# Kernel optimization log

Hardware: AMD Instinct MI355X
Metric: run time of the kernel (lower is better)

The kernel has to match this reference:

```python
import jax, jax.numpy as jnp
import numpy as np

B, L, D = 2, 2048, 1024
H = 16          # num_heads
HD = D // H     # head_dim = 64
NEG_INF = jnp.float32(-1e30)


def setup_inputs() -> dict:
    key = jax.random.key(0)
    ks = jax.random.split(key, 10)
    s = 1.0 / np.sqrt(D)
    return {
        "x": jax.random.normal(ks[0], (B, L, D), dtype=jnp.float32),
        "Wq": jax.random.normal(ks[1], (D, D), dtype=jnp.float32) * s,
        "bq": jnp.zeros((D,), jnp.float32),
        "Wk": jax.random.normal(ks[2], (D, D), dtype=jnp.float32) * s,
        "bk": jnp.zeros((D,), jnp.float32),
        "Wv": jax.random.normal(ks[3], (D, D), dtype=jnp.float32) * s,
        "bv": jnp.zeros((D,), jnp.float32),
        "Wo": jax.random.normal(ks[4], (D, D), dtype=jnp.float32) * s,
        "bo": jnp.zeros((D,), jnp.float32),
        "local_scale": jnp.ones((1,), jnp.float32),
        "global_scale": jnp.ones((1,), jnp.float32),
    }


def reference(x, Wq, bq, Wk, bk, Wv, bv, Wo, bo, local_scale, global_scale):
    # projections -> [B, H, L, HD]
    def proj(W, b):
        return (x @ W + b).reshape(B, L, H, HD).transpose(0, 2, 1, 3)
    Q, K, V = proj(Wq, bq), proj(Wk, bk), proj(Wv, bv)
    lh = H // 2
    inv_sqrt = 1.0 / jnp.sqrt(jnp.float32(HD))

    # local (causal) heads
    scores_l = jnp.einsum("bhqd,bhkd->bhqk", Q[:, :lh], K[:, :lh]) * inv_sqrt
    causal = jnp.tril(jnp.ones((L, L), dtype=bool))  # keep lower triangle
    scores_l = jnp.where(causal, scores_l * local_scale, NEG_INF)
    attn_local = jax.nn.softmax(scores_l, axis=-1)
    out_local = jnp.einsum("bhqk,bhkd->bhqd", attn_local, V[:, :lh])

    # global (full) heads
    scores_g = jnp.einsum("bhqd,bhkd->bhqk", Q[:, lh:], K[:, lh:]) * inv_sqrt
    attn_global = jax.nn.softmax(scores_g * global_scale, axis=-1)
    out_global = jnp.einsum("bhqk,bhkd->bhqd", attn_global, V[:, lh:])

    out = jnp.concatenate([out_local, out_global], axis=1)  # [B,H,L,HD]
    out = out.transpose(0, 2, 1, 3).reshape(B, L, D)
    out = out @ Wo + bo
    return (out, attn_local, attn_global)
```

## Files before the change

### kernel.cpp

```cpp
#include <hip/hip_runtime.h>
#include <hip/hip_bf16.h>

#define B 2
#define L 2048
#define D 1024
#define H 16
#define HD 64
#define LH 8
#define NEG_INF -1e30f

typedef __hip_bfloat16 bf16;
typedef unsigned short ushort_t;
typedef short bf16x8 __attribute__((ext_vector_type(8)));
typedef unsigned short us8 __attribute__((ext_vector_type(8)));
typedef float f32x4 __attribute__((ext_vector_type(4)));

#define MFMA16(a, b, c) __builtin_amdgcn_mfma_f32_16x16x32_bf16((a), (b), (c), 0, 0, 0)

#define WAITBAR(N) do {                                              \
    asm volatile("s_waitcnt vmcnt(" #N ") lgkmcnt(0)" ::: "memory"); \
    __builtin_amdgcn_sched_barrier(0);                               \
    __builtin_amdgcn_s_barrier();                                    \
  } while (0)

#if defined(__has_builtin)
#if __has_builtin(__builtin_amdgcn_global_load_lds)
#define HAVE_GLOAD_LDS 1
#endif
#endif

template<typename T> struct IsF32;
template<> struct IsF32<float> { static constexpr int value = 1; };
template<> struct IsF32<bf16>  { static constexpr int value = 0; };

__device__ __forceinline__ float ldf(const float* p, size_t i) { return p[i]; }
__device__ __forceinline__ float ldf(const bf16* p, size_t i) { return __bfloat162float(p[i]); }

__device__ __forceinline__ float4 ld4(const float* p, size_t i) {
  return *reinterpret_cast<const float4*>(p + i);
}
__device__ __forceinline__ float4 ld4(const bf16* p, size_t i) {
  ushort4 u = *reinterpret_cast<const ushort4*>(p + i);
  float4 f;
  f.x = __uint_as_float(((unsigned)u.x) << 16);
  f.y = __uint_as_float(((unsigned)u.y) << 16);
  f.z = __uint_as_float(((unsigned)u.z) << 16);
  f.w = __uint_as_float(((unsigned)u.w) << 16);
  return f;
}
__device__ __forceinline__ ushort_t bfh(float v) {
  bf16 h = __float2bfloat16(v);
  return *reinterpret_cast<ushort_t*>(&h);
}
__device__ __forceinline__ float bf2f(ushort_t u) {
  return __uint_as_float(((unsigned)u) << 16);
}
__device__ __forceinline__ void stf(float* p, size_t i, float v) { p[i] = v; }
__device__ __forceinline__ void stf(bf16* p, size_t i, float v) { p[i] = __float2bfloat16(v); }

__device__ __forceinline__ int swz(int row, int slot) {
  return row * 64 + (((slot ^ (row & 7)) & 7) << 3);
}
__device__ __forceinline__ int swzc(int row, int c) {
  return row * 64 + (((((c >> 3) ^ row) & 7) << 3) | (c & 7));
}

#if defined(HAVE_GLOAD_LDS)
__device__ __forceinline__ void gload_lds16(const ushort_t* src, ushort_t* dst) {
  __builtin_amdgcn_global_load_lds(
      (const __attribute__((address_space(1))) unsigned int*)src,
      (__attribute__((address_space(3))) unsigned int*)dst, 16, 0, 0);
}
#endif

__device__ __forceinline__ void stage64(const ushort_t* g, size_t gstride,
                                        ushort_t* lds, int w, int ln) {
  #pragma unroll
  for (int c = 0; c < 2; ++c) {
    const int row = 16 * w + 8 * c + (ln >> 3);
    const int slot = ((ln & 7) ^ row) & 7;
    const ushort_t* src = g + (size_t)row * gstride + slot * 8;
#if defined(HAVE_GLOAD_LDS)
    gload_lds16(src, lds + (size_t)(16 * w + 8 * c) * 64);
#else
    *reinterpret_cast<uint4*>(&lds[row * 64 + (ln & 7) * 8]) =
        *reinterpret_cast<const uint4*>(src);
#endif
  }
}

__device__ __forceinline__ void stage128(const ushort_t* g, ushort_t* lds,
                                         int w, int ln) {
  #pragma unroll
  for (int c = 0; c < 4; ++c) {
    const int row = 32 * w + 8 * c + (ln >> 3);
    const int slot = ((ln & 7) ^ row) & 7;
    const ushort_t* src = g + (size_t)row * 1024 + slot * 8;
#if defined(HAVE_GLOAD_LDS)
    gload_lds16(src, lds + (size_t)(32 * w + 8 * c) * 64);
#else
    *reinterpret_cast<uint4*>(&lds[row * 64 + (ln & 7) * 8]) =
        *reinterpret_cast<const uint4*>(src);
#endif
  }
}

__global__ void detect_dtype_kernel(const unsigned short* __restrict__ x,
                                    int* __restrict__ flag) {
  int bad = 0;
  for (int i = threadIdx.x; i < 1024; i += 64) {
    if (((x[i] >> 7) & 0xFF) >= 170) bad = 1;
  }
  unsigned long long m = __ballot(bad);
  if (threadIdx.x == 0) *flag = (m != 0ULL) ? 1 : 0;
}

__global__ __launch_bounds__(256)
void cast_f32_kernel(const int* __restrict__ flag, int want,
                     const float* __restrict__ in,
                     ushort_t* __restrict__ hp, int n4) {
  if (*flag != want) return;
  int i = blockIdx.x * 256 + threadIdx.x;
  const int stride = gridDim.x * 256;
  for (; i < n4; i += stride) {
    float4 v = *reinterpret_cast<const float4*>(in + 4 * (size_t)i);
    ushort4 h;
    h.x = bfh(v.x); h.y = bfh(v.y); h.z = bfh(v.z); h.w = bfh(v.w);
    *reinterpret_cast<ushort4*>(hp + 4 * (size_t)i) = h;
  }
}

template<typename T>
__global__ __launch_bounds__(256)
void transW_kernel(const int* __restrict__ flag,
                   const T* __restrict__ W0, const T* __restrict__ W1,
                   const T* __restrict__ W2, const T* __restrict__ W3,
                   ushort_t* __restrict__ base, ushort_t* __restrict__ baseWo) {
  if (*flag != IsF32<T>::value) return;
  const int z = blockIdx.z;
  const T* W = z == 0 ? W0 : (z == 1 ? W1 : (z == 2 ? W2 : W3));
  ushort_t* hp = (z < 3) ? (base + (size_t)z * 2097152) : baseWo;
  __shared__ float ts[64][69];
  const int k0 = blockIdx.x * 64, n0 = blockIdx.y * 64;
  const int t = threadIdx.x;
  #pragma unroll
  for (int p = 0; p < 4; ++p) {
    int r = p * 16 + (t >> 4);
    int c = (t & 15) * 4;
    float4 v = ld4(W, (size_t)(k0 + r) * D + n0 + c);
    ts[r][c] = v.x; ts[r][c + 1] = v.y; ts[r][c + 2] = v.z; ts[r][c + 3] = v.w;
  }
  __syncthreads();
  #pragma unroll
  for (int p = 0; p < 4; ++p) {
    int n = p * 16 + (t >> 4);
    int k4 = (t & 15) * 4;
    ushort4 h;
    h.x = bfh(ts[k4][n]);
    h.y = bfh(ts[k4 + 1][n]);
    h.z = bfh(ts[k4 + 2][n]);
    h.w = bfh(ts[k4 + 3][n]);
    *reinterpret_cast<ushort4*>(&hp[(size_t)(n0 + n) * D + k0 + k4]) = h;
  }
}

template<typename T>
__global__ __launch_bounds__(256, 3)
void gemm_kernel(const int* __restrict__ flag,
                 const ushort_t* __restrict__ xA, const ushort_t* __restrict__ aoh,
                 const ushort_t* __restrict__ wbase, const ushort_t* __restrict__ woT,
                 const T* __restrict__ bq, const T* __restrict__ bk,
                 const T* __restrict__ bv, const T* __restrict__ bo,
                 ushort_t* __restrict__ qh, ushort_t* __restrict__ ql,
                 ushort_t* __restrict__ kh, ushort_t* __restrict__ kl,
                 ushort_t* __restrict__ vth, T* __restrict__ out0, int zfix) {
  if (*flag != IsF32<T>::value) return;
  const int cpx = gridDim.x >> 3;
  const int swzid = ((int)blockIdx.x & 7) * cpx + ((int)blockIdx.x >> 3);
  const int mtile = swzid & 31;
  const int ntile = (swzid >> 5) & 15;
  const int z = (zfix >= 0) ? zfix : (swzid >> 9);
  const int m0 = mtile * 128, n0 = ntile * 64;

  const bool isOut = (z == 3);
  const ushort_t* Ah = isOut ? aoh : xA;
  const ushort_t* wh = isOut ? woT : (wbase + (size_t)z * 2097152);

  __shared__ ushort_t As[2][8192], Bs[2][4096];

  const int ln = threadIdx.x & 63, w = threadIdx.x >> 6;
  const int m = ln & 15, hi = ln >> 4;

  f32x4 acc[2][4] = {};

  stage128(Ah + (size_t)m0 * 1024, As[0], w, ln);
  stage64(wh + (size_t)n0 * 1024, 1024, Bs[0], w, ln);
  __syncthreads();
  for (int step = 0; step < 16; ++step) {
    const int cur = step & 1;
    if (step < 15) {
      stage128(Ah + (size_t)m0 * 1024 + (step + 1) * 64, As[cur ^ 1], w, ln);
      stage64(wh + (size_t)n0 * 1024 + (step + 1) * 64, 1024, Bs[cur ^ 1], w, ln);
    }
    __builtin_amdgcn_s_setprio(1);
    #pragma unroll
    for (int kc = 0; kc < 2; ++kc) {
      bf16x8 a_h[2], b_h[4];
      #pragma unroll
      for (int f = 0; f < 2; ++f)
        a_h[f] = *reinterpret_cast<const bf16x8*>(&As[cur][swz(w * 32 + f * 16 + m, kc * 4 + hi)]);
      #pragma unroll
      for (int f = 0; f < 4; ++f)
        b_h[f] = *reinterpret_cast<const bf16x8*>(&Bs[cur][swz(f * 16 + m, kc * 4 + hi)]);
      #pragma unroll
      for (int fr = 0; fr < 2; ++fr)
        #pragma unroll
        for (int fc = 0; fc < 4; ++fc)
          acc[fr][fc] = MFMA16(a_h[fr], b_h[fc], acc[fr][fc]);
    }
    __builtin_amdgcn_s_setprio(0);
    __syncthreads();
  }

  #pragma unroll
  for (int fc = 0; fc < 4; ++fc) {
    const int col = n0 + fc * 16 + m;
    if (isOut) {
      const float bv_ = ldf(bo, (size_t)col);
      #pragma unroll
      for (int fr = 0; fr < 2; ++fr)
        #pragma unroll
        for (int r = 0; r < 4; ++r) {
          const int tok = m0 + w * 32 + fr * 16 + 4 * hi + r;
          stf(out0, (size_t)tok * D + col, acc[fr][fc][r] + bv_);
        }
    } else if (z == 2) {
      const int hh = col >> 6, d = col & 63;
      const float bv_ = ldf(bv, (size_t)col);
      #pragma unroll
      for (int fr = 0; fr < 2; ++fr) {
        const int tok0 = m0 + w * 32 + fr * 16 + 4 * hi;
        const int bb = tok0 >> 11, ll = tok0 & (L - 1);
        ushort4 hv;
        hv.x = bfh(acc[fr][fc][0] + bv_);
        hv.y = bfh(acc[fr][fc][1] + bv_);
        hv.z = bfh(acc[fr][fc][2] + bv_);
        hv.w = bfh(acc[fr][fc][3] + bv_);
        *reinterpret_cast<ushort4*>(
            &vth[((size_t)(bb * H + hh) * HD + d) * L + ll]) = hv;
      }
    } else {
      const int hh = col >> 6, d = col & 63;
      const float bv_ = ldf(z == 0 ? bq : bk, (size_t)col);
      ushort_t* oh = z == 0 ? qh : kh;
      ushort_t* ol = z == 0 ? ql : kl;
      #pragma unroll
      for (int fr = 0; fr < 2; ++fr)
        #pragma unroll
        for (int r = 0; r < 4; ++r) {
          const int tok = m0 + w * 32 + fr * 16 + 4 * hi + r;
          const int bb = tok >> 11, ll = tok & (L - 1);
          const float v = acc[fr][fc][r] + bv_;
          const size_t o = ((size_t)(bb * H + hh) * L + ll) * HD + d;
          const ushort_t hu = bfh(v);
          oh[o] = hu; ol[o] = bfh(v - bf2f(hu));
        }
    }
  }
}

template<typename T>
__global__ __launch_bounds__(256, 3)
void attn_kernel(const int* __restrict__ flag,
                 const ushort_t* __restrict__ Qh_g, const ushort_t* __restrict__ Ql_g,
                 const ushort_t* __restrict__ Kh_g, const ushort_t* __restrict__ Kl_g,
                 const ushort_t* __restrict__ Vth_g,
                 const T* __restrict__ lsp, const T* __restrict__ gsp,
                 T* __restrict__ attn_l, T* __restrict__ attn_g,
                 ushort_t* __restrict__ AOh) {
  if (*flag != IsF32<T>::value) return;
  const int bid = blockIdx.x;
  const int xcd = bid & 7, slot = bid >> 3;
  const int bhg = xcd + 8 * (slot >> 5);
  const int strip_raw = slot & 31;
  const int bb = bhg >> 4, h = bhg & 15;
  const bool is_local = h < LH;
  const int strip = is_local ? (31 - strip_raw) : strip_raw;
  const int q0 = strip * 64;
  const int ln = threadIdx.x & 63, w = threadIdx.x >> 6;
  const int m = ln & 15, hi = ln >> 4;

  const float cscale =
      (is_local ? ldf(lsp, (size_t)0) : ldf(gsp, (size_t)0)) * 0.125f;
  const size_t bh_off = ((size_t)bb * H + h) * L * HD;
  const ushort_t* Qhb = Qh_g + bh_off;
  const ushort_t* Qlb = Ql_g + bh_off;
  const ushort_t* Khb = Kh_g + bh_off;
  const ushort_t* Klb = Kl_g + bh_off;
  const ushort_t* Vhb = Vth_g + bh_off;

  __shared__ ushort_t KsH[2][4096], KsL[2][4096], VsH[4096], Ps[4096];

  bf16x8 qfh[2], qfl[2];
  {
    const size_t qb = (size_t)(q0 + 16 * w + m) * HD + hi * 8;
    qfh[0] = *reinterpret_cast<const bf16x8*>(Qhb + qb);
    qfh[1] = *reinterpret_cast<const bf16x8*>(Qhb + qb + 32);
    qfl[0] = *reinterpret_cast<const bf16x8*>(Qlb + qb);
    qfl[1] = *reinterpret_cast<const bf16x8*>(Qlb + qb + 32);
  }

  float m_ = NEG_INF, l_ = 0.f;
  const int nkt = is_local ? (strip + 1) : (L / 64);
  T* aout = is_local ? attn_l : attn_g;
  const size_t arow0 =
      ((size_t)(bb * LH + (is_local ? h : h - LH)) * L + q0) * L;

  stage64(Khb, HD, KsH[0], w, ln);
  __syncthreads();
  for (int kt = 0; kt < nkt; ++kt) {
    const int cur = kt & 1;
    if (kt + 1 < nkt)
      stage64(Khb + (size_t)((kt + 1) * 64) * HD, HD, KsH[cur ^ 1], w, ln);

    f32x4 s[4] = {};
    __builtin_amdgcn_s_setprio(1);
    #pragma unroll
    for (int nt = 0; nt < 4; ++nt) {
      #pragma unroll
      for (int kc = 0; kc < 2; ++kc) {
        bf16x8 kbh = *reinterpret_cast<const bf16x8*>(&KsH[cur][swz(nt * 16 + m, kc * 4 + hi)]);
        s[nt] = MFMA16(kbh, qfh[kc], s[nt]);
      }
    }
    __builtin_amdgcn_s_setprio(0);

    const bool dg = is_local && (kt == strip);
    #pragma unroll
    for (int nt = 0; nt < 4; ++nt)
      #pragma unroll
      for (int r = 0; r < 4; ++r) {
        float v = s[nt][r] * cscale;
        if (dg && (nt * 16 + 4 * hi + r > 16 * w + m)) v = NEG_INF;
        s[nt][r] = v;
      }

    float tm = NEG_INF;
    #pragma unroll
    for (int nt = 0; nt < 4; ++nt)
      #pragma unroll
      for (int r = 0; r < 4; ++r) tm = fmaxf(tm, s[nt][r]);
    tm = fmaxf(tm, __shfl_xor(tm, 16, 64));
    tm = fmaxf(tm, __shfl_xor(tm, 32, 64));
    const float mn = fmaxf(m_, tm);
    float sum = 0.f;
    #pragma unroll
    for (int nt = 0; nt < 4; ++nt)
      #pragma unroll
      for (int r = 0; r < 4; ++r) sum += __expf(s[nt][r] - mn);
    sum += __shfl_xor(sum, 16, 64);
    sum += __shfl_xor(sum, 32, 64);
    l_ = l_ * __expf(m_ - mn) + sum;
    m_ = mn;
    __syncthreads();
  }

  const float invl = 1.0f / l_;
  f32x4 o_[4] = {};

  stage64(Khb, HD, KsH[0], w, ln);
  stage64(Klb, HD, KsL[0], w, ln);
  __syncthreads();
  for (int kt = 0; kt < nkt; ++kt) {
    const int cur = kt & 1;
    const bool pf = (kt + 1 < nkt);
    stage64(Vhb + (size_t)(kt * 64), L, VsH, w, ln);
    if (pf) {
      stage64(Khb + (size_t)((kt + 1) * 64) * HD, HD, KsH[cur ^ 1], w, ln);
      stage64(Klb + (size_t)((kt + 1) * 64) * HD, HD, KsL[cur ^ 1], w, ln);
    }

    f32x4 s[4] = {};
    __builtin_amdgcn_s_setprio(1);
    #pragma unroll
    for (int nt = 0; nt < 4; ++nt) {
      #pragma unroll
      for (int kc = 0; kc < 2; ++kc) {
        bf16x8 kbh = *reinterpret_cast<const bf16x8*>(&KsH[cur][swz(nt * 16 + m, kc * 4 + hi)]);
        bf16x8 kbl = *reinterpret_cast<const bf16x8*>(&KsL[cur][swz(nt * 16 + m, kc * 4 + hi)]);
        s[nt] = MFMA16(kbh, qfh[kc], s[nt]);
        s[nt] = MFMA16(kbl, qfh[kc], s[nt]);
        s[nt] = MFMA16(kbh, qfl[kc], s[nt]);
      }
    }
    __builtin_amdgcn_s_setprio(0);

    const bool dg = is_local && (kt == strip);
    #pragma unroll
    for (int nt = 0; nt < 4; ++nt) {
      float v0 = s[nt][0] * cscale, v1 = s[nt][1] * cscale;
      float v2 = s[nt][2] * cscale, v3 = s[nt][3] * cscale;
      if (dg) {
        const int kbq = nt * 16 + 4 * hi, qq = 16 * w + m;
        if (kbq + 0 > qq) v0 = NEG_INF;
        if (kbq + 1 > qq) v1 = NEG_INF;
        if (kbq + 2 > qq) v2 = NEG_INF;
        if (kbq + 3 > qq) v3 = NEG_INF;
      }
      ushort4 pk;
      pk.x = bfh(__expf(v0 - m_) * invl);
      pk.y = bfh(__expf(v1 - m_) * invl);
      pk.z = bfh(__expf(v2 - m_) * invl);
      pk.w = bfh(__expf(v3 - m_) * invl);
      *reinterpret_cast<ushort4*>(&Ps[swzc(16 * w + m, nt * 16 + 4 * hi)]) = pk;
    }
    if (pf) { WAITBAR(4); } else { WAITBAR(0); }

    __builtin_amdgcn_s_setprio(1);
    bf16x8 pf0 = *reinterpret_cast<const bf16x8*>(&Ps[swz(16 * w + m, hi)]);
    bf16x8 pf1 = *reinterpret_cast<const bf16x8*>(&Ps[swz(16 * w + m, 4 + hi)]);
    #pragma unroll
    for (int dt = 0; dt < 4; ++dt) {
      bf16x8 vf0 = *reinterpret_cast<const bf16x8*>(&VsH[swz(dt * 16 + m, hi)]);
      bf16x8 vf1 = *reinterpret_cast<const bf16x8*>(&VsH[swz(dt * 16 + m, 4 + hi)]);
      o_[dt] = MFMA16(pf0, vf0, o_[dt]);
      o_[dt] = MFMA16(pf1, vf1, o_[dt]);
    }
    __builtin_amdgcn_s_setprio(0);

    {
      const int pr = 16 * w + (ln >> 2);
      const int cs = (ln & 3) * 2;
      us8 v0 = *reinterpret_cast<const us8*>(&Ps[swz(pr, cs)]);
      us8 v1 = *reinterpret_cast<const us8*>(&Ps[swz(pr, cs + 1)]);
      const size_t gi = arow0 + (size_t)pr * L + (size_t)(kt * 64 + (ln & 3) * 16);
      if constexpr (IsF32<T>::value) {
        float* dst = (float*)aout + gi;
        *reinterpret_cast<float4*>(dst + 0) =
            make_float4(bf2f(v0[0]), bf2f(v0[1]), bf2f(v0[2]), bf2f(v0[3]));
        *reinterpret_cast<float4*>(dst + 4) =
            make_float4(bf2f(v0[4]), bf2f(v0[5]), bf2f(v0[6]), bf2f(v0[7]));
        *reinterpret_cast<float4*>(dst + 8) =
            make_float4(bf2f(v1[0]), bf2f(v1[1]), bf2f(v1[2]), bf2f(v1[3]));
        *reinterpret_cast<float4*>(dst + 12) =
            make_float4(bf2f(v1[4]), bf2f(v1[5]), bf2f(v1[6]), bf2f(v1[7]));
      } else {
        bf16* dst = (bf16*)aout + gi;
        *reinterpret_cast<uint4*>(dst + 0) = *reinterpret_cast<const uint4*>(&v0);
        *reinterpret_cast<uint4*>(dst + 8) = *reinterpret_cast<const uint4*>(&v1);
      }
    }
    WAITBAR(4);
  }

  if (is_local) {
    const int pr = 16 * w + (ln >> 2);
    const size_t rbase = arow0 + (size_t)pr * L;
    for (int c = nkt * 64 + (ln & 3) * 16; c < L; c += 64) {
      if constexpr (IsF32<T>::value) {
        float* dst = (float*)aout + rbase + c;
        const float4 z4 = make_float4(0.f, 0.f, 0.f, 0.f);
        *reinterpret_cast<float4*>(dst + 0) = z4;
        *reinterpret_cast<float4*>(dst + 4) = z4;
        *reinterpret_cast<float4*>(dst + 8) = z4;
        *reinterpret_cast<float4*>(dst + 12) = z4;
      } else {
        bf16* dst = (bf16*)aout + rbase + c;
        const uint4 z4 = make_uint4(0u, 0u, 0u, 0u);
        *reinterpret_cast<uint4*>(dst + 0) = z4;
        *reinterpret_cast<uint4*>(dst + 8) = z4;
      }
    }
  }

  #pragma unroll
  for (int dt = 0; dt < 4; ++dt)
    #pragma unroll
    for (int r = 0; r < 4; ++r)
      AOh[((size_t)bb * L + q0 + 16 * w + 4 * hi + r) * D + h * HD + dt * 16 + m] =
          bfh(o_[dt][r]);
}

template<typename T>
static void launch_path(void* const* d_in, void* d_out, void* d_ws, hipStream_t stream) {
  const int want = IsF32<T>::value;
  const int* flag = (const int*)d_ws;
  ushort_t* Qh  = (ushort_t*)((char*)d_ws + 256);
  ushort_t* Ql  = Qh + 4194304;
  ushort_t* Kh  = Ql + 4194304;
  ushort_t* Kl  = Kh + 4194304;
  ushort_t* Vth = Kl + 4194304;
  ushort_t* AOh = Vth + 4194304;
  ushort_t* Woth = AOh + 4194304;

  const T* x  = (const T*)d_in[0];
  const T* Wq = (const T*)d_in[1];
  const T* bq = (const T*)d_in[2];
  const T* Wk = (const T*)d_in[3];
  const T* bk = (const T*)d_in[4];
  const T* Wv = (const T*)d_in[5];
  const T* bv = (const T*)d_in[6];
  const T* Wo = (const T*)d_in[7];
  const T* bo = (const T*)d_in[8];
  const T* ls = (const T*)d_in[9];
  const T* gs = (const T*)d_in[10];

  T* out0   = (T*)d_out;
  T* attn_l = out0 + (size_t)B * L * D;
  T* attn_g = attn_l + (size_t)B * LH * L * L;
  ushort_t* xh  = (ushort_t*)attn_g;
  ushort_t* Wt3 = xh + 4194304;

  if constexpr (IsF32<T>::value)
    cast_f32_kernel<<<1024, 256, 0, stream>>>(flag, want, (const float*)x, xh, 1048576);
  transW_kernel<T><<<dim3(16, 16, 4), 256, 0, stream>>>(
      flag, Wq, Wk, Wv, Wo, Wt3, Woth);
  const ushort_t* xA = IsF32<T>::value ? xh : (const ushort_t*)x;

  gemm_kernel<T><<<1536, 256, 0, stream>>>(
      flag, xA, AOh, Wt3, Woth, bq, bk, bv, bo,
      Qh, Ql, Kh, Kl, Vth, out0, -1);
  attn_kernel<T><<<1024, 256, 0, stream>>>(
      flag, Qh, Ql, Kh, Kl, Vth, ls, gs, attn_l, attn_g, AOh);
  gemm_kernel<T><<<512, 256, 0, stream>>>(
      flag, xA, AOh, Wt3, Woth, bq, bk, bv, bo,
      Qh, Ql, Kh, Kl, Vth, out0, 3);
}

extern "C" void kernel_launch(void* const* d_in, const int* in_sizes, int n_in,
                              void* d_out, int out_size, void* d_ws, size_t ws_size,
                              hipStream_t stream) {
  int* flag = (int*)d_ws;
  detect_dtype_kernel<<<1, 64, 0, stream>>>((const unsigned short*)d_in[0], flag);
  launch_path<float>(d_in, d_out, d_ws, stream);
  launch_path<bf16>(d_in, d_out, d_ws, stream);
}
```

Baseline: 921.1 us.

## Shrink GEMM M-tile to 64 and double-batch K tiles in attention stats pass

The projection GEMMs now use 64x64 tiles instead of 128x64, doubling the grid size and lowering LDS and register use per block; launch bounds are raised to 5 blocks per SM. The attention kernel's shared memory is merged into one aliased buffer. Its first (row-max/sum) pass now stages two K tiles per barrier, halving synchronisations in that pass. Smaller GEMM tiles cut A/B reuse per MFMA, adding more global and LDS traffic in exchange for occupancy.

```diff
diff --git a/kernel.cpp b/kernel.cpp
--- a/kernel.cpp
+++ b/kernel.cpp
@@ -82,22 +82,6 @@
     const ushort_t* src = g + (size_t)row * gstride + slot * 8;
 #if defined(HAVE_GLOAD_LDS)
     gload_lds16(src, lds + (size_t)(16 * w + 8 * c) * 64);
-#else
-    *reinterpret_cast<uint4*>(&lds[row * 64 + (ln & 7) * 8]) =
-        *reinterpret_cast<const uint4*>(src);
-#endif
-  }
-}
-
-__device__ __forceinline__ void stage128(const ushort_t* g, ushort_t* lds,
-                                         int w, int ln) {
-  #pragma unroll
-  for (int c = 0; c < 4; ++c) {
-    const int row = 32 * w + 8 * c + (ln >> 3);
-    const int slot = ((ln & 7) ^ row) & 7;
-    const ushort_t* src = g + (size_t)row * 1024 + slot * 8;
-#if defined(HAVE_GLOAD_LDS)
-    gload_lds16(src, lds + (size_t)(32 * w + 8 * c) * 64);
 #else
     *reinterpret_cast<uint4*>(&lds[row * 64 + (ln & 7) * 8]) =
         *reinterpret_cast<const uint4*>(src);
@@ -165,7 +149,7 @@
 }
 
 template<typename T>
-__global__ __launch_bounds__(256, 3)
+__global__ __launch_bounds__(256, 5)
 void gemm_kernel(const int* __restrict__ flag,
                  const ushort_t* __restrict__ xA, const ushort_t* __restrict__ aoh,
                  const ushort_t* __restrict__ wbase, const ushort_t* __restrict__ woT,
@@ -177,46 +161,42 @@
   if (*flag != IsF32<T>::value) return;
   const int cpx = gridDim.x >> 3;
   const int swzid = ((int)blockIdx.x & 7) * cpx + ((int)blockIdx.x >> 3);
-  const int mtile = swzid & 31;
-  const int ntile = (swzid >> 5) & 15;
-  const int z = (zfix >= 0) ? zfix : (swzid >> 9);
-  const int m0 = mtile * 128, n0 = ntile * 64;
+  const int mtile = swzid & 63;
+  const int ntile = (swzid >> 6) & 15;
+  const int z = (zfix >= 0) ? zfix : (swzid >> 10);
+  const int m0 = mtile * 64, n0 = ntile * 64;
 
   const bool isOut = (z == 3);
   const ushort_t* Ah = isOut ? aoh : xA;
   const ushort_t* wh = isOut ? woT : (wbase + (size_t)z * 2097152);
 
-  __shared__ ushort_t As[2][8192], Bs[2][4096];
+  __shared__ ushort_t As[2][4096], Bs[2][4096];
 
   const int ln = threadIdx.x & 63, w = threadIdx.x >> 6;
   const int m = ln & 15, hi = ln >> 4;
 
-  f32x4 acc[2][4] = {};
-
-  stage128(Ah + (size_t)m0 * 1024, As[0], w, ln);
+  f32x4 acc[4] = {};
+
+  stage64(Ah + (size_t)m0 * 1024, 1024, As[0], w, ln);
   stage64(wh + (size_t)n0 * 1024, 1024, Bs[0], w, ln);
   __syncthreads();
   for (int step = 0; step < 16; ++step) {
     const int cur = step & 1;
     if (step < 15) {
-      stage128(Ah + (size_t)m0 * 1024 + (step + 1) * 64, As[cur ^ 1], w, ln);
+      stage64(Ah + (size_t)m0 * 1024 + (step + 1) * 64, 1024, As[cur ^ 1], w, ln);
       stage64(wh + (size_t)n0 * 1024 + (step + 1) * 64, 1024, Bs[cur ^ 1], w, ln);
     }
     __builtin_amdgcn_s_setprio(1);
     #pragma unroll
     for (int kc = 0; kc < 2; ++kc) {
-      bf16x8 a_h[2], b_h[4];
-      #pragma unroll
-      for (int f = 0; f < 2; ++f)
-        a_h[f] = *reinterpret_cast<const bf16x8*>(&As[cur][swz(w * 32 + f * 16 + m, kc * 4 + hi)]);
+      bf16x8 a_h = *reinterpret_cast<const bf16x8*>(&As[cur][swz(16 * w + m, kc * 4 + hi)]);
+      bf16x8 b_h[4];
       #pragma unroll
       for (int f = 0; f < 4; ++f)
         b_h[f] = *reinterpret_cast<const bf16x8*>(&Bs[cur][swz(f * 16 + m, kc * 4 + hi)]);
       #pragma unroll
-      for (int fr = 0; fr < 2; ++fr)
-        #pragma unroll
-        for (int fc = 0; fc < 4; ++fc)
-          acc[fr][fc] = MFMA16(a_h[fr], b_h[fc], acc[fr][fc]);
+      for (int fc = 0; fc < 4; ++fc)
+        acc[fc] = MFMA16(a_h, b_h[fc], acc[fc]);
     }
     __builtin_amdgcn_s_setprio(0);
     __syncthreads();
@@ -228,43 +208,36 @@
     if (isOut) {
       const float bv_ = ldf(bo, (size_t)col);
       #pragma unroll
-      for (int fr = 0; fr < 2; ++fr)
-        #pragma unroll
-        for (int r = 0; r < 4; ++r) {
-          const int tok = m0 + w * 32 + fr * 16 + 4 * hi + r;
-          stf(out0, (size_t)tok * D + col, acc[fr][fc][r] + bv_);
-        }
+      for (int r = 0; r < 4; ++r) {
+        const int tok = m0 + 16 * w + 4 * hi + r;
+        stf(out0, (size_t)tok * D + col, acc[fc][r] + bv_);
+      }
     } else if (z == 2) {
       const int hh = col >> 6, d = col & 63;
       const float bv_ = ldf(bv, (size_t)col);
-      #pragma unroll
-      for (int fr = 0; fr < 2; ++fr) {
-        const int tok0 = m0 + w * 32 + fr * 16 + 4 * hi;
-        const int bb = tok0 >> 11, ll = tok0 & (L - 1);
-        ushort4 hv;
-        hv.x = bfh(acc[fr][fc][0] + bv_);
-        hv.y = bfh(acc[fr][fc][1] + bv_);
-        hv.z = bfh(acc[fr][fc][2] + bv_);
-        hv.w = bfh(acc[fr][fc][3] + bv_);
-        *reinterpret_cast<ushort4*>(
-            &vth[((size_t)(bb * H + hh) * HD + d) * L + ll]) = hv;
-      }
+      const int tok0 = m0 + 16 * w + 4 * hi;
+      const int bb = tok0 >> 11, ll = tok0 & (L - 1);
+      ushort4 hv;
+      hv.x = bfh(acc[fc][0] + bv_);
+      hv.y = bfh(acc[fc][1] + bv_);
+      hv.z = bfh(acc[fc][2] + bv_);
+      hv.w = bfh(acc[fc][3] + bv_);
+      *reinterpret_cast<ushort4*>(
+          &vth[((size_t)(bb * H + hh) * HD + d) * L + ll]) = hv;
     } else {
       const int hh = col >> 6, d = col & 63;
       const float bv_ = ldf(z == 0 ? bq : bk, (size_t)col);
       ushort_t* oh = z == 0 ? qh : kh;
       ushort_t* ol = z == 0 ? ql : kl;
       #pragma unroll
-      for (int fr = 0; fr < 2; ++fr)
-        #pragma unroll
-        for (int r = 0; r < 4; ++r) {
-          const int tok = m0 + w * 32 + fr * 16 + 4 * hi + r;
-          const int bb = tok >> 11, ll = tok & (L - 1);
-          const float v = acc[fr][fc][r] + bv_;
-          const size_t o = ((size_t)(bb * H + hh) * L + ll) * HD + d;
-          const ushort_t hu = bfh(v);
-          oh[o] = hu; ol[o] = bfh(v - bf2f(hu));
-        }
+      for (int r = 0; r < 4; ++r) {
+        const int tok = m0 + 16 * w + 4 * hi + r;
+        const int bb = tok >> 11, ll = tok & (L - 1);
+        const float v = acc[fc][r] + bv_;
+        const size_t o = ((size_t)(bb * H + hh) * L + ll) * HD + d;
+        const ushort_t hu = bfh(v);
+        oh[o] = hu; ol[o] = bfh(v - bf2f(hu));
+      }
     }
   }
 }
@@ -299,7 +272,9 @@
   const ushort_t* Klb = Kl_g + bh_off;
   const ushort_t* Vhb = Vth_g + bh_off;
 
-  __shared__ ushort_t KsH[2][4096], KsL[2][4096], VsH[4096], Ps[4096];
+  __shared__ ushort_t SH[24576];
+  ushort_t* VsH = SH + 16384;
+  ushort_t* Ps  = SH + 20480;
 
   bf16x8 qfh[2], qfl[2];
   {
@@ -316,83 +291,95 @@
   const size_t arow0 =
       ((size_t)(bb * LH + (is_local ? h : h - LH)) * L + q0) * L;
 
-  stage64(Khb, HD, KsH[0], w, ln);
-  __syncthreads();
-  for (int kt = 0; kt < nkt; ++kt) {
-    const int cur = kt & 1;
-    if (kt + 1 < nkt)
-      stage64(Khb + (size_t)((kt + 1) * 64) * HD, HD, KsH[cur ^ 1], w, ln);
-
-    f32x4 s[4] = {};
-    __builtin_amdgcn_s_setprio(1);
-    #pragma unroll
-    for (int nt = 0; nt < 4; ++nt) {
-      #pragma unroll
-      for (int kc = 0; kc < 2; ++kc) {
-        bf16x8 kbh = *reinterpret_cast<const bf16x8*>(&KsH[cur][swz(nt * 16 + m, kc * 4 + hi)]);
-        s[nt] = MFMA16(kbh, qfh[kc], s[nt]);
-      }
-    }
-    __builtin_amdgcn_s_setprio(0);
-
-    const bool dg = is_local && (kt == strip);
-    #pragma unroll
-    for (int nt = 0; nt < 4; ++nt)
-      #pragma unroll
-      for (int r = 0; r < 4; ++r) {
-        float v = s[nt][r] * cscale;
-        if (dg && (nt * 16 + 4 * hi + r > 16 * w + m)) v = NEG_INF;
-        s[nt][r] = v;
-      }
-
-    float tm = NEG_INF;
-    #pragma unroll
-    for (int nt = 0; nt < 4; ++nt)
-      #pragma unroll
-      for (int r = 0; r < 4; ++r) tm = fmaxf(tm, s[nt][r]);
-    tm = fmaxf(tm, __shfl_xor(tm, 16, 64));
-    tm = fmaxf(tm, __shfl_xor(tm, 32, 64));
-    const float mn = fmaxf(m_, tm);
-    float sum = 0.f;
-    #pragma unroll
-    for (int nt = 0; nt < 4; ++nt)
-      #pragma unroll
-      for (int r = 0; r < 4; ++r) sum += __expf(s[nt][r] - mn);
-    sum += __shfl_xor(sum, 16, 64);
-    sum += __shfl_xor(sum, 32, 64);
-    l_ = l_ * __expf(m_ - mn) + sum;
-    m_ = mn;
+  {
+    const int np = (nkt + 1) >> 1;
+    stage64(Khb, HD, SH, w, ln);
+    if (1 < nkt) stage64(Khb + (size_t)64 * HD, HD, SH + 4096, w, ln);
     __syncthreads();
+    for (int p = 0; p < np; ++p) {
+      ushort_t* base = SH + (p & 1) * 8192;
+      if (p + 1 < np) {
+        ushort_t* nb = SH + ((p + 1) & 1) * 8192;
+        stage64(Khb + (size_t)((2 * p + 2) * 64) * HD, HD, nb, w, ln);
+        if (2 * p + 3 < nkt)
+          stage64(Khb + (size_t)((2 * p + 3) * 64) * HD, HD, nb + 4096, w, ln);
+      }
+      const int nsub = (2 * p + 1 < nkt) ? 2 : 1;
+      #pragma unroll 2
+      for (int sub = 0; sub < nsub; ++sub) {
+        const int kt = 2 * p + sub;
+        const ushort_t* tb = base + sub * 4096;
+        f32x4 s[4] = {};
+        __builtin_amdgcn_s_setprio(1);
+        #pragma unroll
+        for (int nt = 0; nt < 4; ++nt)
+          #pragma unroll
+          for (int kc = 0; kc < 2; ++kc) {
+            bf16x8 kbh = *reinterpret_cast<const bf16x8*>(&tb[swz(nt * 16 + m, kc * 4 + hi)]);
+            s[nt] = MFMA16(kbh, qfh[kc], s[nt]);
+          }
+        __builtin_amdgcn_s_setprio(0);
+
+        const bool dg = is_local && (kt == strip);
+        #pragma unroll
+        for (int nt = 0; nt < 4; ++nt)
+          #pragma unroll
+          for (int r = 0; r < 4; ++r) {
+            float v = s[nt][r] * cscale;
+            if (dg && (nt * 16 + 4 * hi + r > 16 * w + m)) v = NEG_INF;
+            s[nt][r] = v;
+          }
+        float tm = NEG_INF;
+        #pragma unroll
+        for (int nt = 0; nt < 4; ++nt)
+          #pragma unroll
+          for (int r = 0; r < 4; ++r) tm = fmaxf(tm, s[nt][r]);
+        tm = fmaxf(tm, __shfl_xor(tm, 16, 64));
+        tm = fmaxf(tm, __shfl_xor(tm, 32, 64));
+        const float mn = fmaxf(m_, tm);
+        float sum = 0.f;
+        #pragma unroll
+        for (int nt = 0; nt < 4; ++nt)
+          #pragma unroll
+          for (int r = 0; r < 4; ++r) sum += __expf(s[nt][r] - mn);
+        sum += __shfl_xor(sum, 16, 64);
+        sum += __shfl_xor(sum, 32, 64);
+        l_ = l_ * __expf(m_ - mn) + sum;
+        m_ = mn;
+      }
+      __syncthreads();
+    }
   }
 
   const float invl = 1.0f / l_;
   f32x4 o_[4] = {};
 
-  stage64(Khb, HD, KsH[0], w, ln);
-  stage64(Klb, HD, KsL[0], w, ln);
+  stage64(Khb, HD, SH, w, ln);
+  stage64(Klb, HD, SH + 8192, w, ln);
   __syncthreads();
   for (int kt = 0; kt < nkt; ++kt) {
     const int cur = kt & 1;
     const bool pf = (kt + 1 < nkt);
+    ushort_t* KsHc = SH + cur * 4096;
+    ushort_t* KsLc = SH + 8192 + cur * 4096;
     stage64(Vhb + (size_t)(kt * 64), L, VsH, w, ln);
     if (pf) {
-      stage64(Khb + (size_t)((kt + 1) * 64) * HD, HD, KsH[cur ^ 1], w, ln);
-      stage64(Klb + (size_t)((kt + 1) * 64) * HD, HD, KsL[cur ^ 1], w, ln);
+      stage64(Khb + (size_t)((kt + 1) * 64) * HD, HD, SH + (cur ^ 1) * 4096, w, ln);
+      stage64(Klb + (size_t)((kt + 1) * 64) * HD, HD, SH + 8192 + (cur ^ 1) * 4096, w, ln);
     }
 
     f32x4 s[4] = {};
     __builtin_amdgcn_s_setprio(1);
     #pragma unroll
-    for (int nt = 0; nt < 4; ++nt) {
+    for (int nt = 0; nt < 4; ++nt)
       #pragma unroll
       for (int kc = 0; kc < 2; ++kc) {
-        bf16x8 kbh = *reinterpret_cast<const bf16x8*>(&KsH[cur][swz(nt * 16 + m, kc * 4 + hi)]);
-        bf16x8 kbl = *reinterpret_cast<const bf16x8*>(&KsL[cur][swz(nt * 16 + m, kc * 4 + hi)]);
+        bf16x8 kbh = *reinterpret_cast<const bf16x8*>(&KsHc[swz(nt * 16 + m, kc * 4 + hi)]);
+        bf16x8 kbl = *reinterpret_cast<const bf16x8*>(&KsLc[swz(nt * 16 + m, kc * 4 + hi)]);
         s[nt] = MFMA16(kbh, qfh[kc], s[nt]);
         s[nt] = MFMA16(kbl, qfh[kc], s[nt]);
         s[nt] = MFMA16(kbh, qfl[kc], s[nt]);
       }
-    }
     __builtin_amdgcn_s_setprio(0);
 
     const bool dg = is_local && (kt == strip);
@@ -517,12 +504,12 @@
       flag, Wq, Wk, Wv, Wo, Wt3, Woth);
   const ushort_t* xA = IsF32<T>::value ? xh : (const ushort_t*)x;
 
-  gemm_kernel<T><<<1536, 256, 0, stream>>>(
+  gemm_kernel<T><<<3072, 256, 0, stream>>>(
       flag, xA, AOh, Wt3, Woth, bq, bk, bv, bo,
       Qh, Ql, Kh, Kl, Vth, out0, -1);
   attn_kernel<T><<<1024, 256, 0, stream>>>(
       flag, Qh, Ql, Kh, Kl, Vth, ls, gs, attn_l, attn_g, AOh);
-  gemm_kernel<T><<<512, 256, 0, stream>>>(
+  gemm_kernel<T><<<1024, 256, 0, stream>>>(
       flag, xA, AOh, Wt3, Woth, bq, bk, bv, bo,
       Qh, Ql, Kh, Kl, Vth, out0, 3);
 }
```

Result: no change. 918.4 us (-0.3%).
